# Performance work log

Measured on AMD Instinct MI355X. Metric: run time of the kernel, lower is better.

The kernel has to match this reference:

```python
import jax, jax.numpy as jnp
import numpy as np

B, LQ, LK, SIZE, H = 8, 1024, 1024, 512, 8


def setup_inputs() -> dict:
    key = jax.random.key(0)
    ks = jax.random.split(key, 12)
    scale = 1.0 / np.sqrt(SIZE)
    x = jax.random.normal(ks[0], (B, LQ, SIZE), dtype=jnp.float32)
    states = jax.random.normal(ks[1], (B, LK, SIZE), dtype=jnp.float32)
    mask = jax.random.randint(ks[2], (B, LQ, LK), 0, 2, dtype=jnp.int32)
    # Per-head full-size projections, stacked over heads: [H, size, size]
    Wq = jax.random.normal(ks[3], (H, SIZE, SIZE), dtype=jnp.float32) * scale
    bq = jnp.zeros((H, SIZE), dtype=jnp.float32)
    Wk = jax.random.normal(ks[4], (H, SIZE, SIZE), dtype=jnp.float32) * scale
    bk = jnp.zeros((H, SIZE), dtype=jnp.float32)
    Wv = jax.random.normal(ks[5], (H, SIZE, SIZE), dtype=jnp.float32) * scale
    bv = jnp.zeros((H, SIZE), dtype=jnp.float32)
    # Output projection: Linear(size*H, size); torch weight shape [size, size*H]
    Wp = jax.random.normal(ks[6], (SIZE, SIZE * H), dtype=jnp.float32) * (1.0 / np.sqrt(SIZE * H))
    bp = jnp.zeros((SIZE,), dtype=jnp.float32)
    return {"x": x, "states": states, "mask": mask,
            "Wq": Wq, "bq": bq, "Wk": Wk, "bk": bk, "Wv": Wv, "bv": bv,
            "Wp": Wp, "bp": bp}


def reference(x, states, mask, Wq, bq, Wk, bk, Wv, bv, Wp, bp):
    # torch Linear: y = x @ W.T + b ; W is [out,in] so contract over last axis 'e'
    q = jnp.einsum('bqe,hde->bhqd', x, Wq) + bq[:, None, :]       # [B,H,Lq,D]
    k = jnp.einsum('bke,hde->bhkd', states, Wk) + bk[:, None, :]  # [B,H,Lk,D]
    v = jnp.einsum('bke,hde->bhkd', states, Wv) + bv[:, None, :]  # [B,H,Lk,D]
    scores = jnp.einsum('bhqd,bhkd->bhqk', q, k) / jnp.sqrt(jnp.float32(SIZE))
    scores = jnp.where(mask[:, None, :, :] == 0, jnp.float32(-jnp.inf), scores)
    attn = jax.nn.softmax(scores, axis=-1)                        # softmax over Lk
    ctx = jnp.einsum('bhqk,bhkd->bhqd', attn, v)                  # [B,H,Lq,D]
    # concat heads in order -> [B, Lq, H*D]
    ctx = ctx.transpose(0, 2, 1, 3).reshape(B, LQ, H * SIZE)
    return ctx @ Wp.T + bp
```

## Files before the change

### kernel.cpp

```cpp
#include <hip/hip_runtime.h>
#include <hip/hip_bf16.h>

typedef __bf16 bf16_t;
typedef __bf16 bf16x8 __attribute__((ext_vector_type(8)));
typedef float f32x4 __attribute__((ext_vector_type(4)));

#define B_DIM 8
#define LQ 1024
#define LK 1024
#define DD 512
#define NH 8
#define LB 2
#define NCH 4

static __device__ __forceinline__ f32x4 mfma_bf16(bf16x8 a, bf16x8 b, f32x4 c) {
  return __builtin_amdgcn_mfma_f32_16x16x32_bf16(a, b, c, 0, 0, 0);
}

static __device__ __forceinline__ void gld_lds16(const bf16_t* g, bf16_t* l) {
  __builtin_amdgcn_global_load_lds(
      (const __attribute__((address_space(1))) void*)g,
      (__attribute__((address_space(3))) void*)l, 16, 0, 0);
}

__global__ void cvt_pair(const float* __restrict__ s0, bf16_t* __restrict__ d0,
                         const float* __restrict__ s1, bf16_t* __restrict__ d1, int n) {
  const float* s = blockIdx.y ? s1 : s0;
  bf16_t* d = blockIdx.y ? d1 : d0;
  int i = (blockIdx.x * 256 + threadIdx.x) * 4;
  if (i < n) {
    const float4 f = *(const float4*)(s + i);
    bf16_t* p = d + i;
    p[0] = (bf16_t)f.x; p[1] = (bf16_t)f.y; p[2] = (bf16_t)f.z; p[3] = (bf16_t)f.w;
  }
}

__global__ void cvt_w3(const float* __restrict__ s0, const float* __restrict__ s1,
                       const float* __restrict__ s2, bf16_t* __restrict__ d0,
                       bf16_t* __restrict__ d1, bf16_t* __restrict__ d2, int n) {
  const float* s = (blockIdx.y == 0) ? s0 : (blockIdx.y == 1) ? s1 : s2;
  bf16_t* d = (blockIdx.y == 0) ? d0 : (blockIdx.y == 1) ? d1 : d2;
  int i = (blockIdx.x * 256 + threadIdx.x) * 4;
  if (i < n) {
    const float4 f = *(const float4*)(s + i);
    bf16_t* p = d + i;
    p[0] = (bf16_t)f.x; p[1] = (bf16_t)f.y; p[2] = (bf16_t)f.z; p[3] = (bf16_t)f.w;
  }
}

__global__ void cvt_f32_bf16(const float* __restrict__ s, bf16_t* __restrict__ d, int n) {
  int i = (blockIdx.x * 256 + threadIdx.x) * 4;
  if (i < n) {
    const float4 f = *(const float4*)(s + i);
    bf16_t* p = d + i;
    p[0] = (bf16_t)f.x; p[1] = (bf16_t)f.y; p[2] = (bf16_t)f.z; p[3] = (bf16_t)f.w;
  }
}

__global__ void cvt_mask(const int* __restrict__ m, unsigned char* __restrict__ d, int n) {
  int i = (blockIdx.x * 256 + threadIdx.x) * 4;
  if (i < n) {
    const int4 v = *(const int4*)(m + i);
    uchar4 o;
    o.x = (unsigned char)v.x; o.y = (unsigned char)v.y;
    o.z = (unsigned char)v.z; o.w = (unsigned char)v.w;
    *(uchar4*)(d + i) = o;
  }
}

static __device__ __forceinline__ void gemm_core(
    const bf16_t* __restrict__ A, const bf16_t* __restrict__ B, int ld, int klen,
    int m0, int n0, bf16_t* As, bf16_t* Bs, f32x4 (&acc)[4][4])
{
  const int tid = threadIdx.x;
  const int wave = tid >> 6, lane = tid & 63;
  const int l15 = lane & 15, quad = lane >> 4;
  const int wm = (wave & 1) * 64, wn = (wave >> 1) * 64;

  const int r0 = tid >> 3;
  const int c8s = tid & 7;
  bf16_t* Asl = As + tid * 8;
  bf16_t* Bsl = Bs + tid * 8;

  for (int k0 = 0; k0 < klen; k0 += 64) {
    __syncthreads();
#pragma unroll
    for (int p = 0; p < 4; ++p) {
      const int r = r0 + p * 32;
      const int gc = ((c8s ^ (r & 7)) * 8) + k0;
      gld_lds16(A + (size_t)(m0 + r) * ld + gc, Asl + p * 2048);
      gld_lds16(B + (size_t)(n0 + r) * ld + gc, Bsl + p * 2048);
    }
    __syncthreads();
#pragma unroll
    for (int ks = 0; ks < 2; ++ks) {
      bf16x8 af[4], bfr[4];
#pragma unroll
      for (int i = 0; i < 4; ++i) {
        const int r = wm + i * 16 + l15;
        af[i] = *(const bf16x8*)&As[(r * 8 + ((ks * 4 + quad) ^ (r & 7))) * 8];
      }
#pragma unroll
      for (int j = 0; j < 4; ++j) {
        const int r = wn + j * 16 + l15;
        bfr[j] = *(const bf16x8*)&Bs[(r * 8 + ((ks * 4 + quad) ^ (r & 7))) * 8];
      }
#pragma unroll
      for (int i = 0; i < 4; ++i)
#pragma unroll
        for (int j = 0; j < 4; ++j)
          acc[i][j] = mfma_bf16(af[i], bfr[j], acc[i][j]);
    }
  }
}

__global__ __launch_bounds__(256, 4) void gemm_qkv(
    const bf16_t* __restrict__ xcb, const bf16_t* __restrict__ scb,
    const bf16_t* __restrict__ wq, const bf16_t* __restrict__ wk,
    const bf16_t* __restrict__ wv,
    const float* __restrict__ bq, const float* __restrict__ bk,
    const float* __restrict__ bv,
    bf16_t* __restrict__ Qc, bf16_t* __restrict__ Kc, bf16_t* __restrict__ Vtc)
{
  const int role = blockIdx.y >> 4, z = blockIdx.y & 15;
  const int bb = z >> 3, hh = z & 7;
  const int tx = blockIdx.x;

  const bf16_t* A; const bf16_t* Bm; const float* bias; bf16_t* C;
  int m0, n0, ldc, bias_row;
  if (role == 0) {
    A = xcb + (size_t)bb * LQ * DD; Bm = wq + (size_t)hh * DD * DD;
    bias = bq + hh * DD; C = Qc + (size_t)z * LQ * DD;
    m0 = (tx >> 2) * 128; n0 = (tx & 3) * 128; ldc = DD; bias_row = 0;
  } else if (role == 1) {
    A = scb + (size_t)bb * LK * DD; Bm = wk + (size_t)hh * DD * DD;
    bias = bk + hh * DD; C = Kc + (size_t)z * LK * DD;
    m0 = (tx >> 2) * 128; n0 = (tx & 3) * 128; ldc = DD; bias_row = 0;
  } else {
    A = wv + (size_t)hh * DD * DD; Bm = scb + (size_t)bb * LK * DD;
    bias = bv + hh * DD; C = Vtc + (size_t)z * DD * LK;
    m0 = (tx & 3) * 128; n0 = (tx >> 2) * 128; ldc = LK; bias_row = 1;
  }

  __shared__ __align__(16) bf16_t As[128 * 64];
  __shared__ __align__(16) bf16_t Bs[128 * 64];
  f32x4 acc[4][4];
#pragma unroll
  for (int i = 0; i < 4; ++i)
#pragma unroll
    for (int j = 0; j < 4; ++j) acc[i][j] = (f32x4){0.f, 0.f, 0.f, 0.f};

  gemm_core(A, Bm, DD, DD, m0, n0, As, Bs, acc);

  const int tid = threadIdx.x, wave = tid >> 6, lane = tid & 63;
  const int l15 = lane & 15, quad = lane >> 4;
  const int wm = (wave & 1) * 64, wn = (wave >> 1) * 64;
#pragma unroll
  for (int i = 0; i < 4; ++i)
#pragma unroll
    for (int j = 0; j < 4; ++j)
#pragma unroll
      for (int r = 0; r < 4; ++r) {
        const int row = m0 + wm + i * 16 + quad * 4 + r;
        const int col = n0 + wn + j * 16 + l15;
        const float v = acc[i][j][r] + (bias_row ? bias[row] : bias[col]);
        C[(size_t)row * ldc + col] = (bf16_t)v;
      }
}

__global__ __launch_bounds__(256, 4) void gemm_qk(
    const bf16_t* __restrict__ Q, const bf16_t* __restrict__ K,
    const unsigned char* __restrict__ maskb, bf16_t* __restrict__ S,
    float* __restrict__ rs)
{
  const int z = blockIdx.z, bb = z >> 3, nt = blockIdx.y;
  const bf16_t* Az = Q + (size_t)z * LQ * DD;
  const bf16_t* Bz = K + (size_t)z * LK * DD;
  bf16_t* Sz = S + (size_t)z * LQ * LK;
  const unsigned char* mz = maskb + (size_t)bb * LQ * LK;

  const int m0 = blockIdx.x * 128, n0 = nt * 128;
  __shared__ __align__(16) bf16_t As[128 * 64];
  __shared__ __align__(16) bf16_t Bs[128 * 64];
  f32x4 acc[4][4];
#pragma unroll
  for (int i = 0; i < 4; ++i)
#pragma unroll
    for (int j = 0; j < 4; ++j) acc[i][j] = (f32x4){0.f, 0.f, 0.f, 0.f};

  gemm_core(Az, Bz, DD, DD, m0, n0, As, Bs, acc);

  const int tid = threadIdx.x, wave = tid >> 6, lane = tid & 63;
  const int l15 = lane & 15, quad = lane >> 4;
  const int wm = (wave & 1) * 64, wn = (wave >> 1) * 64;
  float* rsz = rs + (((size_t)z * 8 + nt) * 2 + (wave >> 1)) * LQ;
  const float scale = 0.04419417382415922f;

#pragma unroll
  for (int i = 0; i < 4; ++i)
#pragma unroll
    for (int r = 0; r < 4; ++r) {
      const int row = m0 + wm + i * 16 + quad * 4 + r;
      float rsum = 0.f;
#pragma unroll
      for (int j = 0; j < 4; ++j) {
        const int col = n0 + wn + j * 16 + l15;
        const int mv = mz[(size_t)row * LK + col];
        const float p = mv ? __expf(acc[i][j][r] * scale) : 0.f;
        rsum += p;
        Sz[(size_t)row * LK + col] = (bf16_t)p;
      }
      rsum += __shfl_xor(rsum, 1);
      rsum += __shfl_xor(rsum, 2);
      rsum += __shfl_xor(rsum, 4);
      rsum += __shfl_xor(rsum, 8);
      if (l15 == 0) rsz[row] = rsum;
    }
}

__global__ __launch_bounds__(256, 4) void gemm_pv(
    const bf16_t* __restrict__ S, const bf16_t* __restrict__ Vt,
    const float* __restrict__ rs, bf16_t* __restrict__ ctx)
{
  const int z = blockIdx.z, bb = z >> 3, hh = z & 7;
  const bf16_t* Az = S + (size_t)z * LQ * LK;
  const bf16_t* Bz = Vt + (size_t)z * DD * LK;
  bf16_t* Cz = ctx + (size_t)bb * LQ * (NH * DD) + (size_t)hh * DD;

  const int m0 = blockIdx.x * 128, n0 = blockIdx.y * 128;
  __shared__ __align__(16) bf16_t As[128 * 64];
  __shared__ __align__(16) bf16_t Bs[128 * 64];
  __shared__ float invs[128];

  const int tid = threadIdx.x;
  if (tid < 128) {
    const float* p = rs + (size_t)z * 16 * LQ + (m0 + tid);
    float tot = 0.f;
#pragma unroll
    for (int s = 0; s < 16; ++s) tot += p[s * LQ];
    invs[tid] = 1.f / tot;
  }

  f32x4 acc[4][4];
#pragma unroll
  for (int i = 0; i < 4; ++i)
#pragma unroll
    for (int j = 0; j < 4; ++j) acc[i][j] = (f32x4){0.f, 0.f, 0.f, 0.f};

  gemm_core(Az, Bz, LK, LK, m0, n0, As, Bs, acc);

  const int wave = tid >> 6, lane = tid & 63;
  const int l15 = lane & 15, quad = lane >> 4;
  const int wm = (wave & 1) * 64, wn = (wave >> 1) * 64;

#pragma unroll
  for (int i = 0; i < 4; ++i)
#pragma unroll
    for (int r = 0; r < 4; ++r) {
      const int lrow = wm + i * 16 + quad * 4 + r;
      const float iv = invs[lrow];
#pragma unroll
      for (int j = 0; j < 4; ++j) {
        const int col = n0 + wn + j * 16 + l15;
        Cz[(size_t)(m0 + lrow) * (NH * DD) + col] = (bf16_t)(acc[i][j][r] * iv);
      }
    }
}

__global__ __launch_bounds__(256, 4) void gemm_outk(
    const bf16_t* __restrict__ ctx, const bf16_t* __restrict__ wp,
    float* __restrict__ partial)
{
  const int ks = blockIdx.z;
  const bf16_t* A = ctx + ks * 1024;
  const bf16_t* B = wp + ks * 1024;
  float* P = partial + (size_t)ks * B_DIM * LQ * DD;

  const int m0 = blockIdx.x * 128, n0 = blockIdx.y * 128;
  __shared__ __align__(16) bf16_t As[128 * 64];
  __shared__ __align__(16) bf16_t Bs[128 * 64];
  f32x4 acc[4][4];
#pragma unroll
  for (int i = 0; i < 4; ++i)
#pragma unroll
    for (int j = 0; j < 4; ++j) acc[i][j] = (f32x4){0.f, 0.f, 0.f, 0.f};

  gemm_core(A, B, NH * DD, 1024, m0, n0, As, Bs, acc);

  const int tid = threadIdx.x, wave = tid >> 6, lane = tid & 63;
  const int l15 = lane & 15, quad = lane >> 4;
  const int wm = (wave & 1) * 64, wn = (wave >> 1) * 64;
#pragma unroll
  for (int i = 0; i < 4; ++i)
#pragma unroll
    for (int j = 0; j < 4; ++j)
#pragma unroll
      for (int r = 0; r < 4; ++r) {
        const int row = m0 + wm + i * 16 + quad * 4 + r;
        const int col = n0 + wn + j * 16 + l15;
        P[(size_t)row * DD + col] = acc[i][j][r];
      }
}

__global__ void reduce_out(const float* __restrict__ p, const float* __restrict__ bp,
                           float* __restrict__ out) {
  const int N = B_DIM * LQ * DD;
  int i = (blockIdx.x * 256 + threadIdx.x) * 4;
  float4 a = *(const float4*)(p + i);
  float4 b = *(const float4*)(p + N + i);
  float4 c = *(const float4*)(p + 2 * N + i);
  float4 d = *(const float4*)(p + 3 * N + i);
  const float4 bb4 = *(const float4*)(bp + (i & 511));
  float4 r;
  r.x = a.x + b.x + c.x + d.x + bb4.x;
  r.y = a.y + b.y + c.y + d.y + bb4.y;
  r.z = a.z + b.z + c.z + d.z + bb4.z;
  r.w = a.w + b.w + c.w + d.w + bb4.w;
  *(float4*)(out + i) = r;
}

extern "C" void kernel_launch(void* const* d_in, const int* in_sizes, int n_in,
                              void* d_out, int out_size, void* d_ws, size_t ws_size,
                              hipStream_t stream) {
  const float* x      = (const float*)d_in[0];
  const float* states = (const float*)d_in[1];
  const int*   mask   = (const int*)d_in[2];
  const float* Wq     = (const float*)d_in[3];
  const float* bq     = (const float*)d_in[4];
  const float* Wk     = (const float*)d_in[5];
  const float* bk     = (const float*)d_in[6];
  const float* Wv     = (const float*)d_in[7];
  const float* bv     = (const float*)d_in[8];
  const float* Wp     = (const float*)d_in[9];
  const float* bp     = (const float*)d_in[10];
  float* out = (float*)d_out;

  char* ws = (char*)d_ws;
  bf16_t* ctxb = (bf16_t*)(ws + 0);
  bf16_t* wqb  = (bf16_t*)(ws + 67108864);
  bf16_t* wkb  = (bf16_t*)(ws + 71303168);
  bf16_t* wvb  = (bf16_t*)(ws + 75497472);
  bf16_t* Qc   = (bf16_t*)(ws + 79691776);
  bf16_t* Kc   = (bf16_t*)(ws + 96468992);
  bf16_t* Vtc  = (bf16_t*)(ws + 113246208);
  bf16_t* Sb   = (bf16_t*)(ws + 130023424);
  bf16_t* xcb  = (bf16_t*)(ws + 163577856);
  bf16_t* scb  = (bf16_t*)(ws + 165675008);
  bf16_t* wpb  = Qc;
  float*  pbuf = (float*)(ws + 96468992);
  float*  rsum = out;
  unsigned char* mkb = (unsigned char*)out + (1 << 20);

  const int n_w = NH * DD * DD;
  const int n_xc = LB * LQ * DD;
  const int n_mk = LB * LQ * LK;

  cvt_w3<<<dim3(n_w / 1024, 3), 256, 0, stream>>>(Wq, Wk, Wv, wqb, wkb, wvb, n_w);

  for (int c = 0; c < NCH; ++c) {
    const float* xc = x + (size_t)c * LB * LQ * DD;
    const float* sc = states + (size_t)c * LB * LK * DD;
    const int* mc = mask + (size_t)c * LB * LQ * LK;
    bf16_t* ctxc = ctxb + (size_t)c * LB * LQ * (NH * DD);

    cvt_pair<<<dim3(n_xc / 1024, 2), 256, 0, stream>>>(xc, xcb, sc, scb, n_xc);
    cvt_mask<<<n_mk / 1024, 256, 0, stream>>>(mc, mkb, n_mk);

    gemm_qkv<<<dim3(32, 3 * LB * NH), 256, 0, stream>>>(
        xcb, scb, wqb, wkb, wvb, bq, bk, bv, Qc, Kc, Vtc);

    gemm_qk<<<dim3(8, 8, LB * NH), 256, 0, stream>>>(Qc, Kc, mkb, Sb, rsum);
    gemm_pv<<<dim3(8, 4, LB * NH), 256, 0, stream>>>(Sb, Vtc, rsum, ctxc);
  }

  cvt_f32_bf16<<<n_w / 1024, 256, 0, stream>>>(Wp, wpb, n_w);
  gemm_outk<<<dim3(64, 4, 4), 256, 0, stream>>>(ctxb, wpb, pbuf);
  reduce_out<<<(B_DIM * LQ * DD) / 1024, 256, 0, stream>>>(pbuf, bp, out);
}
```

Measured before the change: 594.6 us.

## Swizzle workgroups across XCDs and hoist mask and Wp conversions out of loop

Adds an XCD-aware remapping of the linear workgroup id in all four GEMM kernels, so blocks that share operands (same batch/head) land on the same XCD and can reuse its L2. It also converts the full mask to bytes once instead of per chunk, and converts Wp together with Wq/Wk/Wv in a single launch. Wp now lives in the output buffer so it no longer aliases Qc. The point is to cut launch count and L2 misses. The risk is scratch-space overlap between the mask bytes, the row sums and wpb, which are all placed inside the output buffer.

```diff
diff --git a/kernel.cpp b/kernel.cpp
--- a/kernel.cpp
+++ b/kernel.cpp
@@ -21,6 +21,10 @@
   __builtin_amdgcn_global_load_lds(
       (const __attribute__((address_space(1))) void*)g,
       (__attribute__((address_space(3))) void*)l, 16, 0, 0);
+}
+
+static __device__ __forceinline__ int xcd_swz(int lin, int nwg) {
+  return (lin & 7) * (nwg >> 3) + (lin >> 3);
 }
 
 __global__ void cvt_pair(const float* __restrict__ s0, bf16_t* __restrict__ d0,
@@ -35,20 +39,14 @@
   }
 }
 
-__global__ void cvt_w3(const float* __restrict__ s0, const float* __restrict__ s1,
-                       const float* __restrict__ s2, bf16_t* __restrict__ d0,
-                       bf16_t* __restrict__ d1, bf16_t* __restrict__ d2, int n) {
-  const float* s = (blockIdx.y == 0) ? s0 : (blockIdx.y == 1) ? s1 : s2;
-  bf16_t* d = (blockIdx.y == 0) ? d0 : (blockIdx.y == 1) ? d1 : d2;
-  int i = (blockIdx.x * 256 + threadIdx.x) * 4;
-  if (i < n) {
-    const float4 f = *(const float4*)(s + i);
-    bf16_t* p = d + i;
-    p[0] = (bf16_t)f.x; p[1] = (bf16_t)f.y; p[2] = (bf16_t)f.z; p[3] = (bf16_t)f.w;
-  }
-}
-
-__global__ void cvt_f32_bf16(const float* __restrict__ s, bf16_t* __restrict__ d, int n) {
+__global__ void cvt_w4(const float* __restrict__ s0, const float* __restrict__ s1,
+                       const float* __restrict__ s2, const float* __restrict__ s3,
+                       bf16_t* __restrict__ d0, bf16_t* __restrict__ d1,
+                       bf16_t* __restrict__ d2, bf16_t* __restrict__ d3, int n) {
+  const float* s = (blockIdx.y == 0) ? s0 : (blockIdx.y == 1) ? s1
+                   : (blockIdx.y == 2) ? s2 : s3;
+  bf16_t* d = (blockIdx.y == 0) ? d0 : (blockIdx.y == 1) ? d1
+              : (blockIdx.y == 2) ? d2 : d3;
   int i = (blockIdx.x * 256 + threadIdx.x) * 4;
   if (i < n) {
     const float4 f = *(const float4*)(s + i);
@@ -122,9 +120,11 @@
     const float* __restrict__ bv,
     bf16_t* __restrict__ Qc, bf16_t* __restrict__ Kc, bf16_t* __restrict__ Vtc)
 {
-  const int role = blockIdx.y >> 4, z = blockIdx.y & 15;
+  const int lin = blockIdx.y * 32 + blockIdx.x;
+  const int wg = xcd_swz(lin, 32 * 3 * LB * NH);
+  const int tx = wg & 31, yy = wg >> 5;
+  const int role = yy >> 4, z = yy & 15;
   const int bb = z >> 3, hh = z & 7;
-  const int tx = blockIdx.x;
 
   const bf16_t* A; const bf16_t* Bm; const float* bias; bf16_t* C;
   int m0, n0, ldc, bias_row;
@@ -173,13 +173,16 @@
     const unsigned char* __restrict__ maskb, bf16_t* __restrict__ S,
     float* __restrict__ rs)
 {
-  const int z = blockIdx.z, bb = z >> 3, nt = blockIdx.y;
+  const int lin = (blockIdx.z * 8 + blockIdx.y) * 8 + blockIdx.x;
+  const int wg = xcd_swz(lin, 8 * 8 * LB * NH);
+  const int bx = wg & 7, nt = (wg >> 3) & 7, z = wg >> 6;
+  const int bb = z >> 3;
   const bf16_t* Az = Q + (size_t)z * LQ * DD;
   const bf16_t* Bz = K + (size_t)z * LK * DD;
   bf16_t* Sz = S + (size_t)z * LQ * LK;
   const unsigned char* mz = maskb + (size_t)bb * LQ * LK;
 
-  const int m0 = blockIdx.x * 128, n0 = nt * 128;
+  const int m0 = bx * 128, n0 = nt * 128;
   __shared__ __align__(16) bf16_t As[128 * 64];
   __shared__ __align__(16) bf16_t Bs[128 * 64];
   f32x4 acc[4][4];
@@ -222,12 +225,15 @@
     const bf16_t* __restrict__ S, const bf16_t* __restrict__ Vt,
     const float* __restrict__ rs, bf16_t* __restrict__ ctx)
 {
-  const int z = blockIdx.z, bb = z >> 3, hh = z & 7;
+  const int lin = (blockIdx.z * 4 + blockIdx.y) * 8 + blockIdx.x;
+  const int wg = xcd_swz(lin, 8 * 4 * LB * NH);
+  const int bx = wg & 7, by = (wg >> 3) & 3, z = wg >> 5;
+  const int bb = z >> 3, hh = z & 7;
   const bf16_t* Az = S + (size_t)z * LQ * LK;
   const bf16_t* Bz = Vt + (size_t)z * DD * LK;
   bf16_t* Cz = ctx + (size_t)bb * LQ * (NH * DD) + (size_t)hh * DD;
 
-  const int m0 = blockIdx.x * 128, n0 = blockIdx.y * 128;
+  const int m0 = bx * 128, n0 = by * 128;
   __shared__ __align__(16) bf16_t As[128 * 64];
   __shared__ __align__(16) bf16_t Bs[128 * 64];
   __shared__ float invs[128];
@@ -271,12 +277,14 @@
     const bf16_t* __restrict__ ctx, const bf16_t* __restrict__ wp,
     float* __restrict__ partial)
 {
-  const int ks = blockIdx.z;
+  const int lin = (blockIdx.z * 4 + blockIdx.y) * 64 + blockIdx.x;
+  const int wg = xcd_swz(lin, 1024);
+  const int bx = wg & 63, by = (wg >> 6) & 3, ks = wg >> 8;
   const bf16_t* A = ctx + ks * 1024;
   const bf16_t* B = wp + ks * 1024;
   float* P = partial + (size_t)ks * B_DIM * LQ * DD;
 
-  const int m0 = blockIdx.x * 128, n0 = blockIdx.y * 128;
+  const int m0 = bx * 128, n0 = by * 128;
   __shared__ __align__(16) bf16_t As[128 * 64];
   __shared__ __align__(16) bf16_t Bs[128 * 64];
   f32x4 acc[4][4];
@@ -346,34 +354,34 @@
   bf16_t* Sb   = (bf16_t*)(ws + 130023424);
   bf16_t* xcb  = (bf16_t*)(ws + 163577856);
   bf16_t* scb  = (bf16_t*)(ws + 165675008);
-  bf16_t* wpb  = Qc;
   float*  pbuf = (float*)(ws + 96468992);
   float*  rsum = out;
   unsigned char* mkb = (unsigned char*)out + (1 << 20);
+  bf16_t* wpb  = (bf16_t*)((char*)out + 9 * (1 << 20));
 
   const int n_w = NH * DD * DD;
   const int n_xc = LB * LQ * DD;
-  const int n_mk = LB * LQ * LK;
-
-  cvt_w3<<<dim3(n_w / 1024, 3), 256, 0, stream>>>(Wq, Wk, Wv, wqb, wkb, wvb, n_w);
+  const int n_mk_all = B_DIM * LQ * LK;
+
+  cvt_w4<<<dim3(n_w / 1024, 4), 256, 0, stream>>>(
+      Wq, Wk, Wv, Wp, wqb, wkb, wvb, wpb, n_w);
+  cvt_mask<<<n_mk_all / 1024, 256, 0, stream>>>(mask, mkb, n_mk_all);
 
   for (int c = 0; c < NCH; ++c) {
     const float* xc = x + (size_t)c * LB * LQ * DD;
     const float* sc = states + (size_t)c * LB * LK * DD;
-    const int* mc = mask + (size_t)c * LB * LQ * LK;
+    const unsigned char* mc = mkb + (size_t)c * LB * LQ * LK;
     bf16_t* ctxc = ctxb + (size_t)c * LB * LQ * (NH * DD);
 
     cvt_pair<<<dim3(n_xc / 1024, 2), 256, 0, stream>>>(xc, xcb, sc, scb, n_xc);
-    cvt_mask<<<n_mk / 1024, 256, 0, stream>>>(mc, mkb, n_mk);
 
     gemm_qkv<<<dim3(32, 3 * LB * NH), 256, 0, stream>>>(
         xcb, scb, wqb, wkb, wvb, bq, bk, bv, Qc, Kc, Vtc);
 
-    gemm_qk<<<dim3(8, 8, LB * NH), 256, 0, stream>>>(Qc, Kc, mkb, Sb, rsum);
+    gemm_qk<<<dim3(8, 8, LB * NH), 256, 0, stream>>>(Qc, Kc, mc, Sb, rsum);
     gemm_pv<<<dim3(8, 4, LB * NH), 256, 0, stream>>>(Sb, Vtc, rsum, ctxc);
   }
 
-  cvt_f32_bf16<<<n_w / 1024, 256, 0, stream>>>(Wp, wpb, n_w);
   gemm_outk<<<dim3(64, 4, 4), 256, 0, stream>>>(ctxb, wpb, pbuf);
   reduce_out<<<(B_DIM * LQ * DD) / 1024, 256, 0, stream>>>(pbuf, bp, out);
 }
```

After: 530.9 us. 10.7% less time.
